# Kernel optimization log

Measured on AMD Instinct MI355X. Metric: run time of the kernel, lower is better.

## Reference

```python
import jax, jax.numpy as jnp
import numpy as np

N = 40962          # icosphere level-6 vertex count
E = 245772         # N * k (k=6 knn, directed)
MUL_IN = 8         # '8x0e + 8x1o' -> dim 8 + 24 = 32
MUL_OUT = 16       # '16x0e + 16x1o' -> dim 16 + 48 = 64
H = 64             # radial MLP hidden
WNUM = 4 * MUL_IN * MUL_OUT  # 512 per-edge TP weights (4 CG paths)
SQ3 = np.float32(np.sqrt(3.0))


def setup_inputs() -> dict:
    key = jax.random.key(0)
    ks = jax.random.split(key, 8)
    x = jax.random.normal(ks[0], (N, MUL_IN + 3 * MUL_IN), dtype=jnp.float32)
    pos = jax.random.normal(ks[1], (N, 3), dtype=jnp.float32)
    src = jax.random.randint(ks[2], (E,), 0, N)
    dst = jax.random.randint(ks[3], (E,), 0, N)
    edge_index = jnp.stack([src, dst]).astype(jnp.int32)
    W1 = jax.random.normal(ks[4], (1, H), dtype=jnp.float32)
    W2 = jax.random.normal(ks[5], (H, WNUM), dtype=jnp.float32)
    Ws = jax.random.normal(ks[6], (MUL_OUT, MUL_OUT), dtype=jnp.float32)
    k7, k8 = jax.random.split(ks[7])
    Wns = jax.random.normal(k7, (MUL_OUT, MUL_OUT), dtype=jnp.float32)
    Wg = jax.random.normal(k8, (MUL_OUT, MUL_OUT), dtype=jnp.float32)
    return {"x": x, "pos": pos, "edge_index": edge_index,
            "W1": W1, "W2": W2, "Ws": Ws, "Wns": Wns, "Wg": Wg}


def reference(x, pos, edge_index, W1, W2, Ws, Wns, Wg):
    src, dst = edge_index[0], edge_index[1]
    xs = x[:, :MUL_IN]                                  # (N, 8)  scalars (0e)
    xv = x[:, MUL_IN:].reshape(-1, MUL_IN, 3)           # (N, 8, 3) vectors (1o)

    # --- edge geometry + spherical harmonics (component-normalized, lmax=1) ---
    edge_vec = pos[dst] - pos[src]                      # (E, 3)
    edge_len = jnp.maximum(jnp.linalg.norm(edge_vec, axis=-1, keepdims=True), 1e-8)
    edge_dir = edge_vec / edge_len                      # (E, 3)
    Y1 = SQ3 * edge_dir                                 # l=1 SH; l=0 SH == 1

    # --- radial MLP -> per-edge tensor-product weights (shared_weights=False) ---
    h = jax.nn.silu(edge_len @ W1)                      # (E, H), fan_in = 1
    w = (h @ W2) * (1.0 / np.sqrt(np.float32(H)))       # (E, 512)
    wA, wB, wC, wD = [wi.reshape(-1, MUL_IN, MUL_OUT)
                      for wi in jnp.split(w, 4, axis=1)]

    xs_e = xs[src]                                      # (E, 8)   gather
    xv_e = xv[src]                                      # (E, 8, 3) gather
    norm = np.float32(1.0 / np.sqrt(2.0 * MUL_IN))      # path normalization

    # --- tensor product: 4 CG paths ---
    # 0e x 0e -> 0e  (CG = 1)
    pathA = jnp.einsum('eu,euw->ew', xs_e, wA)
    # 1o x 1o -> 0e  (CG_ij = delta_ij / sqrt(3))
    dot = jnp.einsum('eui,ei->eu', xv_e, Y1) * (1.0 / SQ3)
    pathB = jnp.einsum('eu,euw->ew', dot, wB)
    m_s = (pathA + pathB) * norm                        # (E, 16)
    # 0e x 1o -> 1o  (CG = identity)
    pathC = jnp.einsum('eu,euw->ew', xs_e, wC)[:, :, None] * Y1[:, None, :]
    # 1o x 0e -> 1o  (CG = identity)
    pathD = jnp.einsum('eui,euw->ewi', xv_e, wD)
    m_v = (pathC + pathD) * norm                        # (E, 16, 3)

    m = jnp.concatenate([m_s, m_v.reshape(-1, 3 * MUL_OUT)], axis=1)  # (E, 64)

    # --- scatter-add to destination nodes (index_add) ---
    out = jnp.zeros((x.shape[0], m.shape[1]), dtype=x.dtype).at[dst].add(m)

    # --- gated equivariant nonlinearity (o3.Linear with fan-in norm) ---
    lin_norm = np.float32(1.0 / np.sqrt(np.float32(MUL_OUT)))
    os_ = out[:, :MUL_OUT]                              # (N, 16)
    ov_ = out[:, MUL_OUT:].reshape(-1, MUL_OUT, 3)      # (N, 16, 3)
    s = jax.nn.silu(os_ @ Ws * lin_norm)                # (N, 16)
    ns = jnp.einsum('nui,uw->nwi', ov_, Wns) * lin_norm # (N, 16, 3)
    g = jax.nn.sigmoid(os_ @ Wg * lin_norm)             # (N, 16)
    gated = (g[:, :, None] * ns).reshape(-1, 3 * MUL_OUT)
    return jnp.concatenate([s, gated], axis=1)          # (N, 64)
```

## Files before the change

kernel.cpp:

```cpp
#include <hip/hip_runtime.h>
#include <math.h>

typedef _Float16 half8 __attribute__((ext_vector_type(8)));
typedef float floatx4 __attribute__((ext_vector_type(4)));

#define SQ3 1.7320508075688772f

__global__ __launch_bounds__(256) void prep_w2(const float* __restrict__ W2,
                                               _Float16* __restrict__ bw) {
    int t = blockIdx.x * 256 + threadIdx.x;
    if (t >= 32768) return;
    int i    = t & 7;
    int l    = (t >> 3) & 63;
    int s    = (t >> 9) & 1;
    int tt   = (t >> 10) & 7;
    int path = t >> 13;
    int k   = s * 32 + (l >> 4) * 8 + i;
    int col = path * 128 + tt * 16 + (l & 15);
    float scale = 0.03125f * (path == 2 ? SQ3 : 1.0f);
    bw[t] = (_Float16)(W2[k * 512 + col] * scale);
}

__global__ __launch_bounds__(256) void edge_kernel(
    const float* __restrict__ x, const float* __restrict__ pos,
    const int* __restrict__ ei, const float* __restrict__ W1,
    const _Float16* __restrict__ bw, float* __restrict__ out,
    int E, int ntiles)
{
    __shared__ float sW1[64];
    __shared__ float s_len[16];
    __shared__ float s_dir[16][3];
    __shared__ int   s_src[16];
    __shared__ int   s_dst[16];
    __shared__ __align__(16) float s_xs[16][8];
    __shared__ __align__(16) float s_xv[16][24];
    __shared__ __align__(16) _Float16 s_hA[2][64][8];
    __shared__ float s_ms[2][16][16];
    __shared__ float s_mv[2][16][48];

    const int tid  = threadIdx.x;
    const int wave = tid >> 6;
    const int lane = tid & 63;

    if (tid < 64) sW1[tid] = W1[tid];

    half8 bfrag[8][2];
    {
        const half8* bsrc = (const half8*)bw;
        #pragma unroll
        for (int t = 0; t < 8; ++t)
            #pragma unroll
            for (int s = 0; s < 2; ++s)
                bfrag[t][s] = bsrc[(size_t)wave * 1024 + (t * 2 + s) * 64 + lane];
    }

    for (int tile = blockIdx.x; tile < ntiles; tile += gridDim.x) {
        const int ebase = tile * 16;
        __syncthreads();

        if (tid < 16) {
            int eg = ebase + tid;
            int ec = (eg < E) ? eg : (E - 1);
            int si = ei[ec];
            int di = ei[E + ec];
            s_src[tid] = si;
            s_dst[tid] = di;
            float ex = pos[di * 3 + 0] - pos[si * 3 + 0];
            float ey = pos[di * 3 + 1] - pos[si * 3 + 1];
            float ez = pos[di * 3 + 2] - pos[si * 3 + 2];
            float len = sqrtf(ex * ex + ey * ey + ez * ez);
            len = fmaxf(len, 1e-8f);
            float inv = 1.0f / len;
            s_len[tid] = len;
            s_dir[tid][0] = ex * inv;
            s_dir[tid][1] = ey * inv;
            s_dir[tid][2] = ez * inv;
        }
        __syncthreads();

        if (tid < 128) {
            int e = tid >> 3, q = tid & 7;
            float4 v = *reinterpret_cast<const float4*>(
                x + (size_t)s_src[e] * 32 + q * 4);
            if (q < 2) {
                s_xs[e][q * 4 + 0] = v.x; s_xs[e][q * 4 + 1] = v.y;
                s_xs[e][q * 4 + 2] = v.z; s_xs[e][q * 4 + 3] = v.w;
            } else {
                int b = (q - 2) * 4;
                s_xv[e][b + 0] = v.x; s_xv[e][b + 1] = v.y;
                s_xv[e][b + 2] = v.z; s_xv[e][b + 3] = v.w;
            }
        }
        {
            int slot = tid >> 1;
            int s = slot >> 6;
            int l = slot & 63;
            int e = l & 15;
            int half4 = (tid & 1) * 4;
            int jb = s * 32 + (l >> 4) * 8 + half4;
            float len = s_len[e];
            #pragma unroll
            for (int i = 0; i < 4; ++i) {
                float z = len * sW1[jb + i];
                float h = z / (1.0f + __expf(-z));
                s_hA[s][l][half4 + i] = (_Float16)h;
            }
        }
        __syncthreads();

        half8 a0 = *(const half8*)&s_hA[0][lane][0];
        half8 a1 = *(const half8*)&s_hA[1][lane][0];
        floatx4 acc[8];
        #pragma unroll
        for (int t = 0; t < 8; ++t) {
            floatx4 z = {0.f, 0.f, 0.f, 0.f};
            z = __builtin_amdgcn_mfma_f32_16x16x32_f16(a0, bfrag[t][0], z, 0, 0, 0);
            acc[t] = __builtin_amdgcn_mfma_f32_16x16x32_f16(a1, bfrag[t][1], z, 0, 0, 0);
        }

        const int wp = lane & 15;
        const int er0 = (lane >> 4) * 4;

        if (wave == 0) {
            #pragma unroll
            for (int r = 0; r < 4; ++r) {
                int e = er0 + r;
                float xss[8];
                #pragma unroll
                for (int q = 0; q < 2; ++q) {
                    float4 v = *(const float4*)&s_xs[e][q * 4];
                    xss[q*4+0]=v.x; xss[q*4+1]=v.y; xss[q*4+2]=v.z; xss[q*4+3]=v.w;
                }
                float m = 0.f;
                #pragma unroll
                for (int u = 0; u < 8; ++u) m += xss[u] * acc[u][r];
                s_ms[0][e][wp] = m;
            }
        } else if (wave == 1) {
            #pragma unroll
            for (int r = 0; r < 4; ++r) {
                int e = er0 + r;
                float xvv[24];
                #pragma unroll
                for (int q = 0; q < 6; ++q) {
                    float4 v = *(const float4*)&s_xv[e][q * 4];
                    xvv[q*4+0]=v.x; xvv[q*4+1]=v.y; xvv[q*4+2]=v.z; xvv[q*4+3]=v.w;
                }
                float d0 = s_dir[e][0], d1 = s_dir[e][1], d2 = s_dir[e][2];
                float m = 0.f;
                #pragma unroll
                for (int u = 0; u < 8; ++u) {
                    float dot = xvv[u*3+0]*d0 + xvv[u*3+1]*d1 + xvv[u*3+2]*d2;
                    m += dot * acc[u][r];
                }
                s_ms[1][e][wp] = m;
            }
        } else if (wave == 2) {
            #pragma unroll
            for (int r = 0; r < 4; ++r) {
                int e = er0 + r;
                float xss[8];
                #pragma unroll
                for (int q = 0; q < 2; ++q) {
                    float4 v = *(const float4*)&s_xs[e][q * 4];
                    xss[q*4+0]=v.x; xss[q*4+1]=v.y; xss[q*4+2]=v.z; xss[q*4+3]=v.w;
                }
                float cw = 0.f;
                #pragma unroll
                for (int u = 0; u < 8; ++u) cw += xss[u] * acc[u][r];
                s_mv[0][e][wp * 3 + 0] = cw * s_dir[e][0];
                s_mv[0][e][wp * 3 + 1] = cw * s_dir[e][1];
                s_mv[0][e][wp * 3 + 2] = cw * s_dir[e][2];
            }
        } else {
            #pragma unroll
            for (int r = 0; r < 4; ++r) {
                int e = er0 + r;
                float xvv[24];
                #pragma unroll
                for (int q = 0; q < 6; ++q) {
                    float4 v = *(const float4*)&s_xv[e][q * 4];
                    xvv[q*4+0]=v.x; xvv[q*4+1]=v.y; xvv[q*4+2]=v.z; xvv[q*4+3]=v.w;
                }
                float m0 = 0.f, m1 = 0.f, m2 = 0.f;
                #pragma unroll
                for (int u = 0; u < 8; ++u) {
                    float w = acc[u][r];
                    m0 += xvv[u*3+0] * w;
                    m1 += xvv[u*3+1] * w;
                    m2 += xvv[u*3+2] * w;
                }
                s_mv[1][e][wp * 3 + 0] = m0;
                s_mv[1][e][wp * 3 + 1] = m1;
                s_mv[1][e][wp * 3 + 2] = m2;
            }
        }
        __syncthreads();

        {
            int c  = tid & 63;
            int g  = tid >> 6;
            #pragma unroll
            for (int k = 0; k < 4; ++k) {
                int e  = g * 4 + k;
                int eg = ebase + e;
                if (eg < E) {
                    float v;
                    if (c < 16) v = s_ms[0][e][c] + s_ms[1][e][c];
                    else        v = s_mv[0][e][c - 16] + s_mv[1][e][c - 16];
                    atomicAdd(out + (size_t)s_dst[e] * 64 + c, v);
                }
            }
        }
    }
}

__global__ __launch_bounds__(256) void node_kernel(
    float* __restrict__ out, const float* __restrict__ Ws,
    const float* __restrict__ Wns, const float* __restrict__ Wg, int N)
{
    int n = blockIdx.x * 256 + threadIdx.x;
    if (n >= N) return;
    float* row = out + (size_t)n * 64;

    float os[16], ov[48];
    #pragma unroll
    for (int q = 0; q < 4; ++q) {
        float4 v = *reinterpret_cast<const float4*>(row + q * 4);
        os[q*4+0]=v.x; os[q*4+1]=v.y; os[q*4+2]=v.z; os[q*4+3]=v.w;
    }
    #pragma unroll
    for (int q = 0; q < 12; ++q) {
        float4 v = *reinterpret_cast<const float4*>(row + 16 + q * 4);
        ov[q*4+0]=v.x; ov[q*4+1]=v.y; ov[q*4+2]=v.z; ov[q*4+3]=v.w;
    }

    float sres[16], gres[16];
    #pragma unroll
    for (int w = 0; w < 16; ++w) {
        float a = 0.f, b = 0.f;
        #pragma unroll
        for (int u = 0; u < 16; ++u) {
            float o_u = os[u];
            a += o_u * Ws[u * 16 + w];
            b += o_u * Wg[u * 16 + w];
        }
        a *= 0.25f; b *= 0.25f;
        sres[w] = a / (1.0f + __expf(-a));
        gres[w] = 1.0f / (1.0f + __expf(-b));
    }

    float gated[48];
    #pragma unroll
    for (int w = 0; w < 16; ++w) {
        float n0 = 0.f, n1 = 0.f, n2 = 0.f;
        #pragma unroll
        for (int u = 0; u < 16; ++u) {
            float wn = Wns[u * 16 + w];
            n0 += ov[u*3+0] * wn;
            n1 += ov[u*3+1] * wn;
            n2 += ov[u*3+2] * wn;
        }
        float gw = gres[w] * 0.25f;
        gated[w*3+0] = n0 * gw;
        gated[w*3+1] = n1 * gw;
        gated[w*3+2] = n2 * gw;
    }

    #pragma unroll
    for (int q = 0; q < 4; ++q) {
        float4 v = make_float4(sres[q*4+0], sres[q*4+1], sres[q*4+2], sres[q*4+3]);
        *reinterpret_cast<float4*>(row + q * 4) = v;
    }
    #pragma unroll
    for (int q = 0; q < 12; ++q) {
        float4 v = make_float4(gated[q*4+0], gated[q*4+1], gated[q*4+2], gated[q*4+3]);
        *reinterpret_cast<float4*>(row + 16 + q * 4) = v;
    }
}

extern "C" void kernel_launch(void* const* d_in, const int* in_sizes, int n_in,
                              void* d_out, int out_size, void* d_ws, size_t ws_size,
                              hipStream_t stream) {
    const float* x   = (const float*)d_in[0];
    const float* pos = (const float*)d_in[1];
    const int*   ei  = (const int*)d_in[2];
    const float* W1  = (const float*)d_in[3];
    const float* W2  = (const float*)d_in[4];
    const float* Ws  = (const float*)d_in[5];
    const float* Wns = (const float*)d_in[6];
    const float* Wg  = (const float*)d_in[7];

    int N = in_sizes[0] / 32;
    int E = in_sizes[2] / 2;
    int ntiles = (E + 15) / 16;
    float* out = (float*)d_out;
    _Float16* bw = (_Float16*)d_ws;

    hipMemsetAsync(d_out, 0, (size_t)N * 64 * sizeof(float), stream);
    prep_w2<<<128, 256, 0, stream>>>(W2, bw);
    int nblk = ntiles < 1536 ? ntiles : 1536;
    edge_kernel<<<nblk, 256, 0, stream>>>(x, pos, ei, W1, bw, out, E, ntiles);
    node_kernel<<<(N + 255) / 256, 256, 0, stream>>>(out, Ws, Wns, Wg, N);
}
```

Before: 121.4 us.

## Process 64 edges per tile with fp16 staging and merged geometry/radial stage

Each loop iteration now handles 64 edges instead of 16, so every wave runs four MFMA sub-tiles per synchronisation round, which spreads the barrier and setup cost over more edges. Gathered node features and the per-path partial messages are stored in shared memory as fp16, which cuts LDS footprint and traffic. The geometry, gather and radial SiLU stages are merged into one phase with one barrier fewer per tile, and the grid cap is lowered. In exchange, x and the partial messages lose precision, which may push error against the reference up, and each block holds more shared memory.

```diff
diff --git a/kernel.cpp b/kernel.cpp
--- a/kernel.cpp
+++ b/kernel.cpp
@@ -27,22 +27,19 @@
     const _Float16* __restrict__ bw, float* __restrict__ out,
     int E, int ntiles)
 {
-    __shared__ float sW1[64];
-    __shared__ float s_len[16];
-    __shared__ float s_dir[16][3];
-    __shared__ int   s_src[16];
-    __shared__ int   s_dst[16];
-    __shared__ __align__(16) float s_xs[16][8];
-    __shared__ __align__(16) float s_xv[16][24];
-    __shared__ __align__(16) _Float16 s_hA[2][64][8];
-    __shared__ float s_ms[2][16][16];
-    __shared__ float s_mv[2][16][48];
+    __shared__ __align__(16) float4 sW1v[16];
+    __shared__ __align__(16) float4 s_geo[64];
+    __shared__ int s_dst[64];
+    __shared__ __align__(16) _Float16 s_xs[64][8];
+    __shared__ __align__(16) _Float16 s_xv[64][24];
+    __shared__ __align__(16) _Float16 s_hA[4][2][64][8];
+    __shared__ __align__(16) _Float16 s_part[2][64][64];
 
     const int tid  = threadIdx.x;
     const int wave = tid >> 6;
     const int lane = tid & 63;
 
-    if (tid < 64) sW1[tid] = W1[tid];
+    if (tid < 16) sW1v[tid] = reinterpret_cast<const float4*>(W1)[tid];
 
     half8 bfrag[8][2];
     {
@@ -55,159 +52,157 @@
     }
 
     for (int tile = blockIdx.x; tile < ntiles; tile += gridDim.x) {
-        const int ebase = tile * 16;
+        const int ebase = tile * 64;
         __syncthreads();
 
-        if (tid < 16) {
-            int eg = ebase + tid;
+        {
+            int eg_l = tid >> 2, q = tid & 3;
+            int eg = ebase + eg_l;
             int ec = (eg < E) ? eg : (E - 1);
             int si = ei[ec];
+            const float* xr = x + (size_t)si * 32 + q * 8;
+            float4 va = *reinterpret_cast<const float4*>(xr);
+            float4 vb = *reinterpret_cast<const float4*>(xr + 4);
+            half8 hv;
+            hv[0] = (_Float16)va.x; hv[1] = (_Float16)va.y;
+            hv[2] = (_Float16)va.z; hv[3] = (_Float16)va.w;
+            hv[4] = (_Float16)vb.x; hv[5] = (_Float16)vb.y;
+            hv[6] = (_Float16)vb.z; hv[7] = (_Float16)vb.w;
+            if (q == 0) *(half8*)&s_xs[eg_l][0] = hv;
+            else        *(half8*)&s_xv[eg_l][(q - 1) * 8] = hv;
+        }
+        {
+            int sub = tid >> 6;
+            int l   = tid & 63;
+            int el  = sub * 16 + (l & 15);
+            int kg  = l >> 4;
+            int eg  = ebase + el;
+            int ec  = (eg < E) ? eg : (E - 1);
+            int si = ei[ec];
             int di = ei[E + ec];
-            s_src[tid] = si;
-            s_dst[tid] = di;
             float ex = pos[di * 3 + 0] - pos[si * 3 + 0];
             float ey = pos[di * 3 + 1] - pos[si * 3 + 1];
             float ez = pos[di * 3 + 2] - pos[si * 3 + 2];
             float len = sqrtf(ex * ex + ey * ey + ez * ez);
             len = fmaxf(len, 1e-8f);
             float inv = 1.0f / len;
-            s_len[tid] = len;
-            s_dir[tid][0] = ex * inv;
-            s_dir[tid][1] = ey * inv;
-            s_dir[tid][2] = ez * inv;
+            if (kg == 0) {
+                s_geo[el] = make_float4(ex * inv, ey * inv, ez * inv, len);
+                s_dst[el] = di;
+            }
+            #pragma unroll
+            for (int s = 0; s < 2; ++s) {
+                float4 w0 = sW1v[s * 8 + kg * 2 + 0];
+                float4 w1 = sW1v[s * 8 + kg * 2 + 1];
+                float ww[8] = {w0.x, w0.y, w0.z, w0.w, w1.x, w1.y, w1.z, w1.w};
+                half8 ha;
+                #pragma unroll
+                for (int i = 0; i < 8; ++i) {
+                    float z = len * ww[i];
+                    ha[i] = (_Float16)(z / (1.0f + __expf(-z)));
+                }
+                *(half8*)&s_hA[sub][s][l][0] = ha;
+            }
         }
         __syncthreads();
 
-        if (tid < 128) {
-            int e = tid >> 3, q = tid & 7;
-            float4 v = *reinterpret_cast<const float4*>(
-                x + (size_t)s_src[e] * 32 + q * 4);
-            if (q < 2) {
-                s_xs[e][q * 4 + 0] = v.x; s_xs[e][q * 4 + 1] = v.y;
-                s_xs[e][q * 4 + 2] = v.z; s_xs[e][q * 4 + 3] = v.w;
+        const int wp  = lane & 15;
+        const int er0 = (lane >> 4) * 4;
+        #pragma unroll
+        for (int sub = 0; sub < 4; ++sub) {
+            half8 a0 = *(const half8*)&s_hA[sub][0][lane][0];
+            half8 a1 = *(const half8*)&s_hA[sub][1][lane][0];
+            floatx4 acc[8];
+            #pragma unroll
+            for (int t = 0; t < 8; ++t) {
+                floatx4 z = {0.f, 0.f, 0.f, 0.f};
+                z = __builtin_amdgcn_mfma_f32_16x16x32_f16(a0, bfrag[t][0], z, 0, 0, 0);
+                acc[t] = __builtin_amdgcn_mfma_f32_16x16x32_f16(a1, bfrag[t][1], z, 0, 0, 0);
+            }
+
+            if (wave == 0) {
+                #pragma unroll
+                for (int r = 0; r < 4; ++r) {
+                    int e = sub * 16 + er0 + r;
+                    half8 xs = *(const half8*)&s_xs[e][0];
+                    float m = 0.f;
+                    #pragma unroll
+                    for (int u = 0; u < 8; ++u) m += (float)xs[u] * acc[u][r];
+                    s_part[0][e][wp] = (_Float16)m;
+                }
+            } else if (wave == 1) {
+                #pragma unroll
+                for (int r = 0; r < 4; ++r) {
+                    int e = sub * 16 + er0 + r;
+                    half8 v0 = *(const half8*)&s_xv[e][0];
+                    half8 v1 = *(const half8*)&s_xv[e][8];
+                    half8 v2 = *(const half8*)&s_xv[e][16];
+                    float4 g = s_geo[e];
+                    float xf[24];
+                    #pragma unroll
+                    for (int i = 0; i < 8; ++i) {
+                        xf[i] = (float)v0[i]; xf[8 + i] = (float)v1[i];
+                        xf[16 + i] = (float)v2[i];
+                    }
+                    float m = 0.f;
+                    #pragma unroll
+                    for (int u = 0; u < 8; ++u) {
+                        float dot = xf[u*3+0]*g.x + xf[u*3+1]*g.y + xf[u*3+2]*g.z;
+                        m += dot * acc[u][r];
+                    }
+                    s_part[1][e][wp] = (_Float16)m;
+                }
+            } else if (wave == 2) {
+                #pragma unroll
+                for (int r = 0; r < 4; ++r) {
+                    int e = sub * 16 + er0 + r;
+                    half8 xs = *(const half8*)&s_xs[e][0];
+                    float4 g = s_geo[e];
+                    float cw = 0.f;
+                    #pragma unroll
+                    for (int u = 0; u < 8; ++u) cw += (float)xs[u] * acc[u][r];
+                    s_part[0][e][16 + wp * 3 + 0] = (_Float16)(cw * g.x);
+                    s_part[0][e][16 + wp * 3 + 1] = (_Float16)(cw * g.y);
+                    s_part[0][e][16 + wp * 3 + 2] = (_Float16)(cw * g.z);
+                }
             } else {
-                int b = (q - 2) * 4;
-                s_xv[e][b + 0] = v.x; s_xv[e][b + 1] = v.y;
-                s_xv[e][b + 2] = v.z; s_xv[e][b + 3] = v.w;
-            }
-        }
+                #pragma unroll
+                for (int r = 0; r < 4; ++r) {
+                    int e = sub * 16 + er0 + r;
+                    half8 v0 = *(const half8*)&s_xv[e][0];
+                    half8 v1 = *(const half8*)&s_xv[e][8];
+                    half8 v2 = *(const half8*)&s_xv[e][16];
+                    float xf[24];
+                    #pragma unroll
+                    for (int i = 0; i < 8; ++i) {
+                        xf[i] = (float)v0[i]; xf[8 + i] = (float)v1[i];
+                        xf[16 + i] = (float)v2[i];
+                    }
+                    float m0 = 0.f, m1 = 0.f, m2 = 0.f;
+                    #pragma unroll
+                    for (int u = 0; u < 8; ++u) {
+                        float w = acc[u][r];
+                        m0 += xf[u*3+0] * w;
+                        m1 += xf[u*3+1] * w;
+                        m2 += xf[u*3+2] * w;
+                    }
+                    s_part[1][e][16 + wp * 3 + 0] = (_Float16)m0;
+                    s_part[1][e][16 + wp * 3 + 1] = (_Float16)m1;
+                    s_part[1][e][16 + wp * 3 + 2] = (_Float16)m2;
+                }
+            }
+        }
+        __syncthreads();
+
         {
-            int slot = tid >> 1;
-            int s = slot >> 6;
-            int l = slot & 63;
-            int e = l & 15;
-            int half4 = (tid & 1) * 4;
-            int jb = s * 32 + (l >> 4) * 8 + half4;
-            float len = s_len[e];
+            int c = tid & 63;
+            int g = tid >> 6;
             #pragma unroll
-            for (int i = 0; i < 4; ++i) {
-                float z = len * sW1[jb + i];
-                float h = z / (1.0f + __expf(-z));
-                s_hA[s][l][half4 + i] = (_Float16)h;
-            }
-        }
-        __syncthreads();
-
-        half8 a0 = *(const half8*)&s_hA[0][lane][0];
-        half8 a1 = *(const half8*)&s_hA[1][lane][0];
-        floatx4 acc[8];
-        #pragma unroll
-        for (int t = 0; t < 8; ++t) {
-            floatx4 z = {0.f, 0.f, 0.f, 0.f};
-            z = __builtin_amdgcn_mfma_f32_16x16x32_f16(a0, bfrag[t][0], z, 0, 0, 0);
-            acc[t] = __builtin_amdgcn_mfma_f32_16x16x32_f16(a1, bfrag[t][1], z, 0, 0, 0);
-        }
-
-        const int wp = lane & 15;
-        const int er0 = (lane >> 4) * 4;
-
-        if (wave == 0) {
-            #pragma unroll
-            for (int r = 0; r < 4; ++r) {
-                int e = er0 + r;
-                float xss[8];
-                #pragma unroll
-                for (int q = 0; q < 2; ++q) {
-                    float4 v = *(const float4*)&s_xs[e][q * 4];
-                    xss[q*4+0]=v.x; xss[q*4+1]=v.y; xss[q*4+2]=v.z; xss[q*4+3]=v.w;
-                }
-                float m = 0.f;
-                #pragma unroll
-                for (int u = 0; u < 8; ++u) m += xss[u] * acc[u][r];
-                s_ms[0][e][wp] = m;
-            }
-        } else if (wave == 1) {
-            #pragma unroll
-            for (int r = 0; r < 4; ++r) {
-                int e = er0 + r;
-                float xvv[24];
-                #pragma unroll
-                for (int q = 0; q < 6; ++q) {
-                    float4 v = *(const float4*)&s_xv[e][q * 4];
-                    xvv[q*4+0]=v.x; xvv[q*4+1]=v.y; xvv[q*4+2]=v.z; xvv[q*4+3]=v.w;
-                }
-                float d0 = s_dir[e][0], d1 = s_dir[e][1], d2 = s_dir[e][2];
-                float m = 0.f;
-                #pragma unroll
-                for (int u = 0; u < 8; ++u) {
-                    float dot = xvv[u*3+0]*d0 + xvv[u*3+1]*d1 + xvv[u*3+2]*d2;
-                    m += dot * acc[u][r];
-                }
-                s_ms[1][e][wp] = m;
-            }
-        } else if (wave == 2) {
-            #pragma unroll
-            for (int r = 0; r < 4; ++r) {
-                int e = er0 + r;
-                float xss[8];
-                #pragma unroll
-                for (int q = 0; q < 2; ++q) {
-                    float4 v = *(const float4*)&s_xs[e][q * 4];
-                    xss[q*4+0]=v.x; xss[q*4+1]=v.y; xss[q*4+2]=v.z; xss[q*4+3]=v.w;
-                }
-                float cw = 0.f;
-                #pragma unroll
-                for (int u = 0; u < 8; ++u) cw += xss[u] * acc[u][r];
-                s_mv[0][e][wp * 3 + 0] = cw * s_dir[e][0];
-                s_mv[0][e][wp * 3 + 1] = cw * s_dir[e][1];
-                s_mv[0][e][wp * 3 + 2] = cw * s_dir[e][2];
-            }
-        } else {
-            #pragma unroll
-            for (int r = 0; r < 4; ++r) {
-                int e = er0 + r;
-                float xvv[24];
-                #pragma unroll
-                for (int q = 0; q < 6; ++q) {
-                    float4 v = *(const float4*)&s_xv[e][q * 4];
-                    xvv[q*4+0]=v.x; xvv[q*4+1]=v.y; xvv[q*4+2]=v.z; xvv[q*4+3]=v.w;
-                }
-                float m0 = 0.f, m1 = 0.f, m2 = 0.f;
-                #pragma unroll
-                for (int u = 0; u < 8; ++u) {
-                    float w = acc[u][r];
-                    m0 += xvv[u*3+0] * w;
-                    m1 += xvv[u*3+1] * w;
-                    m2 += xvv[u*3+2] * w;
-                }
-                s_mv[1][e][wp * 3 + 0] = m0;
-                s_mv[1][e][wp * 3 + 1] = m1;
-                s_mv[1][e][wp * 3 + 2] = m2;
-            }
-        }
-        __syncthreads();
-
-        {
-            int c  = tid & 63;
-            int g  = tid >> 6;
-            #pragma unroll
-            for (int k = 0; k < 4; ++k) {
-                int e  = g * 4 + k;
+            for (int k = 0; k < 16; ++k) {
+                int e  = g * 16 + k;
                 int eg = ebase + e;
                 if (eg < E) {
-                    float v;
-                    if (c < 16) v = s_ms[0][e][c] + s_ms[1][e][c];
-                    else        v = s_mv[0][e][c - 16] + s_mv[1][e][c - 16];
+                    float v = (float)s_part[0][e][c] + (float)s_part[1][e][c];
                     atomicAdd(out + (size_t)s_dst[e] * 64 + c, v);
                 }
             }
@@ -293,13 +288,13 @@
 
     int N = in_sizes[0] / 32;
     int E = in_sizes[2] / 2;
-    int ntiles = (E + 15) / 16;
+    int ntiles = (E + 63) / 64;
     float* out = (float*)d_out;
     _Float16* bw = (_Float16*)d_ws;
 
     hipMemsetAsync(d_out, 0, (size_t)N * 64 * sizeof(float), stream);
     prep_w2<<<128, 256, 0, stream>>>(W2, bw);
-    int nblk = ntiles < 1536 ? ntiles : 1536;
+    int nblk = ntiles < 1280 ? ntiles : 1280;
     edge_kernel<<<nblk, 256, 0, stream>>>(x, pos, ei, W1, bw, out, E, ntiles);
     node_kernel<<<(N + 255) / 256, 256, 0, stream>>>(out, Ws, Wns, Wg, N);
 }
```

Result: slower. 127.2 us (+4.8%).
